# Kernel tuning notes

Hardware: AMD Instinct MI355X
Metric: run time of the kernel (lower is better)

The kernel has to match this reference:

```python
import jax, jax.numpy as jnp
import numpy as np

# Loihi neuron constants (from a typical slayerSNN network.yaml)
I_DECAY = 1024.0   # current decay (of 4096)
V_DECAY = 128.0    # voltage decay (of 4096)
THETA = 100.0      # firing threshold


def spike_loihi(x):
    """Loihi CUBA neuron dynamics over trailing time axis. x: [..., T] weighted input."""
    xT = jnp.moveaxis(x, -1, 0)  # [T, ...]
    a_i = (4096.0 - I_DECAY) / 4096.0
    a_v = (4096.0 - V_DECAY) / 4096.0

    def step(carry, xt):
        u, v = carry
        u = a_i * u + xt           # synaptic current
        v = a_v * v + u            # membrane voltage
        s = (v >= THETA).astype(x.dtype)
        v = v * (1.0 - s)          # reset on spike
        return (u, v), s

    z = jnp.zeros(xT.shape[1:], x.dtype)
    _, s = jax.lax.scan(step, (z, z), xT)
    return jnp.moveaxis(s, 0, -1)


def delay_shift(x):
    """Shift spikes by 1 timestep along last axis (slayer.delayShift(spike, 1))."""
    return jnp.concatenate([jnp.zeros_like(x[..., :1]), x[..., :-1]], axis=-1)


def conv_t(x, w):
    """Per-timestep 2D conv, padding 1. x: [N,C,H,W,T], w: [O,I,3,3]."""
    N, C, H, W, T = x.shape
    xt = jnp.transpose(x, (0, 4, 1, 2, 3)).reshape(N * T, C, H, W)
    y = jax.lax.conv_general_dilated(xt, w, (1, 1), [(1, 1), (1, 1)],
                                     dimension_numbers=('NCHW', 'OIHW', 'NCHW'))
    O = w.shape[0]
    return jnp.transpose(y.reshape(N, T, O, H, W), (0, 2, 3, 4, 1))


def sum_pool2(x, w):
    """slayer.pool(2): 2x2 sum-pool scaled by (loaded) scalar pool weight."""
    N, C, H, W, T = x.shape
    return x.reshape(N, C, H // 2, 2, W // 2, 2, T).sum(axis=(3, 5)) * w


def setup_inputs() -> dict:
    key = jax.random.key(0)
    ks = jax.random.split(key, 8)
    N, T = 16, 128
    spike = jax.random.bernoulli(ks[0], 0.1, (N, 2, 40, 40, T)).astype(jnp.float32)
    conv1_w = jax.random.normal(ks[1], (8, 2, 3, 3), jnp.float32) * 0.5
    conv2_w = jax.random.normal(ks[2], (16, 8, 3, 3), jnp.float32) * 0.05
    conv3_w = jax.random.normal(ks[3], (32, 16, 3, 3), jnp.float32) * 0.05
    fc1_w = jax.random.normal(ks[4], (512, 10 * 10 * 32), jnp.float32) * 0.02
    pool1_w = jnp.asarray(1.1, jnp.float32)
    pool2_w = jnp.asarray(1.1, jnp.float32)
    return {"spike": spike, "conv1_w": conv1_w, "conv2_w": conv2_w,
            "conv3_w": conv3_w, "pool1_w": pool1_w, "pool2_w": pool2_w,
            "fc1_w": fc1_w}


def reference(spike, conv1_w, conv2_w, conv3_w, pool1_w, pool2_w, fc1_w):
    x = spike_loihi(conv_t(spike, conv1_w * 20.0))    # weightScale=20
    x = delay_shift(x)
    x = spike_loihi(sum_pool2(x, pool1_w))
    x = delay_shift(x)
    x = spike_loihi(conv_t(x, conv2_w * 100.0))       # weightScale=100
    x = delay_shift(x)
    x = spike_loihi(sum_pool2(x, pool2_w))
    x = delay_shift(x)
    x = spike_loihi(conv_t(x, conv3_w * 100.0))       # weightScale=100
    N, T = x.shape[0], x.shape[-1]
    x = x.reshape(N, -1, 1, 1, T)                     # [N, 3200, 1, 1, T]
    x = delay_shift(x)
    x = spike_loihi(jnp.einsum('nchwt,oc->nohwt', x, fc1_w))
    x = delay_shift(x)
    return x
```

## Files before the change

kernel.cpp:

```cpp
#include <hip/hip_runtime.h>
#include <stdint.h>


#define T 128
#define AI 0.75f
#define AV 0.96875f
#define THETA 100.0f

typedef __attribute__((ext_vector_type(8))) short v8s;
typedef __attribute__((ext_vector_type(16))) float v16f;

__device__ __forceinline__ void neuron_step(float x, float& u, float& v, float& s) {
    u = AI * u + x;
    v = AV * v + u;
    s = (v >= THETA) ? 1.0f : 0.0f;
    v = v * (1.0f - s);
}

__global__ __launch_bounds__(256) void conv1_scan(
    const float* __restrict__ in, const float* __restrict__ cw,
    uint8_t* __restrict__ sout)
{
    __shared__ float ldsF[64 * 130];
    int bid0 = blockIdx.x;
    int bid = (bid0 & 7) * 400 + (bid0 >> 3);
    int wg = bid % 5;
    int hy = (bid / 5) % 40;
    int n  = bid / 200;
    int tid = threadIdx.x;
    int wxl = tid >> 5, tt = tid & 31, t0 = tt * 4;
    int wx = wg * 8 + wxl;

    float4 tap[18];
    #pragma unroll
    for (int c = 0; c < 2; c++)
      #pragma unroll
      for (int dh = 0; dh < 3; dh++)
        #pragma unroll
        for (int dw = 0; dw < 3; dw++) {
            int q = c * 9 + dh * 3 + dw;
            int hh = hy + dh - 1, ww = wx + dw - 1;
            bool ok = (hh >= 0) && (hh < 40) && (ww >= 0) && (ww < 40);
            tap[q] = ok ? *(const float4*)(in +
                (((size_t)(n * 2 + c) * 40 + hh) * 40 + ww) * T + t0)
                        : make_float4(0.f, 0.f, 0.f, 0.f);
        }

    #pragma unroll
    for (int o = 0; o < 8; o++) {
        const float* wp = cw + o * 18;
        float a0 = 0.f, a1 = 0.f, a2 = 0.f, a3 = 0.f;
        #pragma unroll
        for (int q = 0; q < 18; q++) {
            a0 += wp[q] * tap[q].x;  a1 += wp[q] * tap[q].y;
            a2 += wp[q] * tap[q].z;  a3 += wp[q] * tap[q].w;
        }
        float* xr = &ldsF[(o * 8 + wxl) * 130 + t0];
        xr[0] = a0 * 20.0f; xr[1] = a1 * 20.0f;
        xr[2] = a2 * 20.0f; xr[3] = a3 * 20.0f;
    }
    __syncthreads();
    if (tid < 64) {
        int o = tid >> 3, wxl2 = tid & 7;
        float u = 0.f, v = 0.f;
        uint32_t ob[32];
        const float* xr = &ldsF[tid * 130];
        #pragma unroll
        for (int tb = 0; tb < 32; tb++) {
            float s0, s1, s2, s3;
            neuron_step(xr[tb * 4 + 0], u, v, s0);
            neuron_step(xr[tb * 4 + 1], u, v, s1);
            neuron_step(xr[tb * 4 + 2], u, v, s2);
            neuron_step(xr[tb * 4 + 3], u, v, s3);
            ob[tb] = (uint32_t)s0 | ((uint32_t)s1 << 8) |
                     ((uint32_t)s2 << 16) | ((uint32_t)s3 << 24);
        }
        uint32_t* op = (uint32_t*)(sout +
            (((size_t)(n * 8 + o) * 40 + hy) * 40 + wg * 8 + wxl2) * T);
        #pragma unroll
        for (int k = 0; k < 8; k++)
            *(uint4*)&op[k * 4] =
                make_uint4(ob[k*4], ob[k*4+1], ob[k*4+2], ob[k*4+3]);
    }
}

template<int C, int HO, int WO>
__global__ __launch_bounds__(320) void pool_pad(
    const uint8_t* __restrict__ in, const float* __restrict__ pw_ptr,
    uint16_t* __restrict__ sP)
{
    constexpr int CB = 320 / C;
    constexpr int GP = (HO * WO) / CB;
    __shared__ uint8_t raw[320 * 132];
    uint32_t* ldsF = (uint32_t*)raw;
    uint8_t*  sbuf = raw;

    int bid = blockIdx.x;
    int grp = bid % GP, n = bid / GP;
    int tid = threadIdx.x;
    float pw = pw_ptr[0];

    float u = 0.f, v = 0.f;
    uint32_t ob[32];
    uint32_t carry = 0;

    #pragma unroll
    for (int tb = 0; tb < 2; tb++) {
        __syncthreads();
        #pragma unroll
        for (int k = 0; k < 4; k++) {
            int f = tid + k * 320;
            int row = f >> 2, q = f & 3;
            int c = row / CB, p = row % CB;
            int hw = grp * CB + p;
            int wx = hw % WO, hy = hw / WO;
            const uint8_t* p00 = in +
                (((size_t)(n * C + c) * (2 * HO) + 2 * hy) * (2 * WO) + 2 * wx) * T;
            int off = tb * 64 + q * 16;
            uint4 a = *(const uint4*)(p00 + off);
            uint4 b = *(const uint4*)(p00 + T + off);
            uint4 cc = *(const uint4*)(p00 + 2 * WO * T + off);
            uint4 d = *(const uint4*)(p00 + 2 * WO * T + T + off);
            *(uint4*)&ldsF[row * 20 + q * 4] =
                make_uint4(a.x + b.x + cc.x + d.x, a.y + b.y + cc.y + d.y,
                           a.z + b.z + cc.z + d.z, a.w + b.w + cc.w + d.w);
        }
        __syncthreads();
        #pragma unroll
        for (int q = 0; q < 4; q++) {
            uint4 w = *(const uint4*)&ldsF[tid * 20 + q * 4];
            uint32_t words[4] = {w.x, w.y, w.z, w.w};
            #pragma unroll
            for (int j = 0; j < 4; j++) {
                uint32_t cur = words[j];
                uint32_t del = (cur << 8) | carry;
                carry = cur >> 24;
                float s0, s1, s2, s3;
                neuron_step(pw * (float)(del & 0xffu),         u, v, s0);
                neuron_step(pw * (float)((del >> 8) & 0xffu),  u, v, s1);
                neuron_step(pw * (float)((del >> 16) & 0xffu), u, v, s2);
                neuron_step(pw * (float)((del >> 24) & 0xffu), u, v, s3);
                ob[tb * 16 + q * 4 + j] = (uint32_t)s0 | ((uint32_t)s1 << 8) |
                                          ((uint32_t)s2 << 16) | ((uint32_t)s3 << 24);
            }
        }
    }

    __syncthreads();
    #pragma unroll
    for (int j = 0; j < 32; j++)
        *(uint32_t*)&sbuf[tid * 132 + j * 4] = ob[j];
    __syncthreads();

    constexpr int CHK = CB * 128;
    #pragma unroll
    for (int k = 0; k < CHK / 320; k++) {
        int ci = k * 320 + tid;
        int p = ci >> 7, tau = ci & 127;
        int hw = grp * CB + p;
        int wx = hw % WO, hy = hw / WO;
        uint32_t wb[8];
        #pragma unroll
        for (int e = 0; e < 16; e += 2) {
            uint32_t lo = 0u, hi = 0u;
            if (tau >= 1) {
                if (e < C)     lo = sbuf[(e * CB + p) * 132 + tau - 1] ? 0x3F80u : 0u;
                if (e + 1 < C) hi = sbuf[((e + 1) * CB + p) * 132 + tau - 1] ? 0x3F80u : 0u;
            }
            wb[e >> 1] = lo | (hi << 16);
        }
        uint16_t* dst = sP + ((size_t)((n * (HO + 2) + hy + 1) * (WO + 2)
                                       + wx + 1)) * 2048 + tau * 16;
        *(uint4*)dst       = make_uint4(wb[0], wb[1], wb[2], wb[3]);
        *(uint4*)(dst + 8) = make_uint4(wb[4], wb[5], wb[6], wb[7]);
    }
}

template<int H, int W>
__global__ __launch_bounds__(256) void zero_halo(uint16_t* __restrict__ sP)
{
    constexpr int CELLS = (H + 2) * (W + 2);
    int bid = blockIdx.x;
    int cell = bid % CELLS;
    int hy = cell / (W + 2), wx = cell % (W + 2);
    if (hy >= 1 && hy <= H && wx >= 1 && wx <= W) return;
    *(uint4*)((uint8_t*)sP + (size_t)bid * 4096 + threadIdx.x * 16) =
        make_uint4(0u, 0u, 0u, 0u);
}

__global__ __launch_bounds__(64) void apack_w(
    const float* __restrict__ c2w, const float* __restrict__ c3w,
    uint16_t* __restrict__ apk)
{
    int bid = blockIdx.x;
    int conv = bid / 27;
    int plane = (bid % 27) / 9;
    int dlt = bid % 9;
    int lane = threadIdx.x;
    int o = lane & 31, chi = (lane >> 5) * 8;
    int CO = conv ? 32 : 16;
    int CI = conv ? 16 : 8;
    const float* Wp = conv ? c3w : c2w;
    uint32_t wb[4] = {0u, 0u, 0u, 0u};
    #pragma unroll
    for (int e = 0; e < 8; e++) {
        int c = chi + e;
        float w = (o < CO && c < CI) ? Wp[((size_t)o * CI + c) * 9 + dlt] : 0.f;
        uint32_t b0 = __float_as_uint(w);
        uint16_t hi = (uint16_t)(b0 >> 16);
        float r1 = w - __uint_as_float(b0 & 0xFFFF0000u);
        uint32_t b1 = __float_as_uint(r1);
        uint16_t md = (uint16_t)(b1 >> 16);
        float r2 = r1 - __uint_as_float(b1 & 0xFFFF0000u);
        uint16_t lo = (uint16_t)(__float_as_uint(r2) >> 16);
        uint32_t pv = (plane == 0) ? hi : ((plane == 1) ? md : lo);
        wb[e >> 1] |= pv << ((e & 1) * 16);
    }
    *(uint4*)(apk + ((size_t)conv * 27 + plane * 9 + dlt) * 512 + lane * 8) =
        make_uint4(wb[0], wb[1], wb[2], wb[3]);
}

template<int COUT, int PB, int H, int W>
__global__ __launch_bounds__(256, 2) void conv_scan_mfma(
    const uint16_t* __restrict__ sP, const uint16_t* __restrict__ apk,
    float scale, uint8_t* __restrict__ sout)
{
    __shared__ float ldsF[128 * 130];
    constexpr int HW = H * W;
    constexpr int GP = HW / PB;
    int per = (16 * GP) >> 3;
    int vbid = (blockIdx.x & 7) * per + (blockIdx.x >> 3);
    int n = vbid / GP, grp = vbid % GP;
    int tid = threadIdx.x;
    int wv = tid >> 6, lane = tid & 63;
    int l31 = lane & 31, lhi = lane >> 5;
    int t0 = wv * 32;

    const uint16_t* ap = apk + (size_t)lane * 8;
    v8s a0[9], a1[9], a2[9];
    #pragma unroll
    for (int d = 0; d < 9; d++) {
        a0[d] = *(const v8s*)(ap + d * 512);
        a1[d] = *(const v8s*)(ap + (9 + d) * 512);
        a2[d] = *(const v8s*)(ap + (18 + d) * 512);
    }

    #pragma unroll
    for (int p = 0; p < PB; p++) {
        int hw = grp * PB + p;
        int hy = hw / W, wx = hw % W;
        v8s bfr[9];
        #pragma unroll
        for (int d = 0; d < 9; d++) {
            int dh = d / 3, dw = d % 3;
            const uint16_t* src = sP
                + ((size_t)((n * (H + 2) + hy + dh) * (W + 2) + wx + dw)) * 2048
                + (t0 + l31) * 16 + lhi * 8;
            bfr[d] = *(const v8s*)src;
        }
        v16f ac0, ac1, ac2;
        #pragma unroll
        for (int e = 0; e < 16; e++) { ac0[e] = 0.f; ac1[e] = 0.f; ac2[e] = 0.f; }
        #pragma unroll
        for (int d = 0; d < 9; d++) {
            ac0 = __builtin_amdgcn_mfma_f32_32x32x16_bf16(a0[d], bfr[d], ac0, 0, 0, 0);
            ac1 = __builtin_amdgcn_mfma_f32_32x32x16_bf16(a1[d], bfr[d], ac1, 0, 0, 0);
            ac2 = __builtin_amdgcn_mfma_f32_32x32x16_bf16(a2[d], bfr[d], ac2, 0, 0, 0);
        }
        constexpr int NR = (COUT == 32) ? 16 : 8;
        #pragma unroll
        for (int r = 0; r < NR; r++) {
            int o = (r & 3) + 8 * (r >> 2) + 4 * lhi;
            ldsF[(o * PB + p) * 130 + t0 + l31] =
                (ac0[r] + ac1[r] + ac2[r]) * scale;
        }
    }
    __syncthreads();
    if (tid < 128) {
        int o = tid / PB, p = tid % PB;
        int hw = grp * PB + p;
        float u = 0.f, v = 0.f;
        uint32_t ob[32];
        const float* xr = &ldsF[tid * 130];
        #pragma unroll
        for (int tb = 0; tb < 32; tb++) {
            float2 xa = *(const float2*)(xr + tb * 4);
            float2 xb = *(const float2*)(xr + tb * 4 + 2);
            float s0, s1, s2, s3;
            neuron_step(xa.x, u, v, s0); neuron_step(xa.y, u, v, s1);
            neuron_step(xb.x, u, v, s2); neuron_step(xb.y, u, v, s3);
            ob[tb] = (uint32_t)s0 | ((uint32_t)s1 << 8) |
                     ((uint32_t)s2 << 16) | ((uint32_t)s3 << 24);
        }
        uint32_t* op = (uint32_t*)(sout + ((size_t)(n * COUT + o) * HW + hw) * 128);
        #pragma unroll
        for (int k = 0; k < 8; k++)
            *(uint4*)&op[k * 4] =
                make_uint4(ob[k*4], ob[k*4+1], ob[k*4+2], ob[k*4+3]);
    }
}

__global__ __launch_bounds__(256) void wsplit(
    const float* __restrict__ fw, uint16_t* __restrict__ bs)
{
    int i = blockIdx.x * 256 + threadIdx.x;
    float4 wv = *(const float4*)(fw + i * 4);
    float w4[4] = {wv.x, wv.y, wv.z, wv.w};
    uint16_t h[4], m[4], l[4];
    #pragma unroll
    for (int j = 0; j < 4; j++) {
        uint32_t b0 = __float_as_uint(w4[j]);
        h[j] = (uint16_t)(b0 >> 16);
        float r1 = w4[j] - __uint_as_float(b0 & 0xFFFF0000u);
        uint32_t b1 = __float_as_uint(r1);
        m[j] = (uint16_t)(b1 >> 16);
        float r2 = r1 - __uint_as_float(b1 & 0xFFFF0000u);
        l[j] = (uint16_t)(__float_as_uint(r2) >> 16);
    }
    *(ushort4*)(bs +       0 + i * 4) = make_ushort4(h[0], h[1], h[2], h[3]);
    *(ushort4*)(bs + 1638400 + i * 4) = make_ushort4(m[0], m[1], m[2], m[3]);
    *(ushort4*)(bs + 3276800 + i * 4) = make_ushort4(l[0], l[1], l[2], l[3]);
}

__global__ __launch_bounds__(256) void sT_bf16(
    const uint8_t* __restrict__ s5, uint16_t* __restrict__ At)
{
    __shared__ uint8_t tile[64 * 132];
    int bid = blockIdx.x;
    int n = bid / 50;
    int c0 = (bid % 50) * 64;
    int tid = threadIdx.x;
    {
        int row = tid >> 2, q = tid & 3;
        const uint8_t* src = s5 + ((size_t)(n * 3200 + c0 + row)) * T + q * 32;
        *(uint4*)&tile[row * 132 + q * 32]      = *(const uint4*)src;
        *(uint4*)&tile[row * 132 + q * 32 + 16] = *(const uint4*)(src + 16);
    }
    __syncthreads();
    int t = tid >> 1, half = tid & 1;
    uint32_t wb[16];
    if (t == 0) {
        #pragma unroll
        for (int j = 0; j < 16; j++) wb[j] = 0u;
    } else {
        #pragma unroll
        for (int j = 0; j < 16; j++) {
            uint32_t lo = tile[(half * 32 + 2 * j) * 132 + (t - 1)] ? 0x3F80u : 0u;
            uint32_t hi = tile[(half * 32 + 2 * j + 1) * 132 + (t - 1)] ? 0x3F80u : 0u;
            wb[j] = lo | (hi << 16);
        }
    }
    uint16_t* dst = At + ((size_t)(n * 128 + t)) * 3200 + c0 + half * 32;
    #pragma unroll
    for (int k = 0; k < 4; k++)
        *(uint4*)(dst + k * 8) = make_uint4(wb[k*4], wb[k*4+1], wb[k*4+2], wb[k*4+3]);
}

#define GLDS16(g, s) __builtin_amdgcn_global_load_lds( \
    (const __attribute__((address_space(1))) uint32_t*)(g), \
    (__attribute__((address_space(3))) uint32_t*)(s), 16, 0, 0)

__global__ __launch_bounds__(256, 2) void fc_gemm_mfma(
    const uint16_t* __restrict__ At,
    const uint16_t* __restrict__ Bs,
    float* __restrict__ ypart)
{
    __shared__ uint8_t lds[65536];
    int bid0 = blockIdx.x;
    int bid = (bid0 & 7) * 80 + (bid0 >> 3);
    int n  = bid & 15;
    int ob = (bid >> 4) & 3;
    int ks = bid >> 6;
    int o0 = ob * 128;
    int cbase = ks * 320;

    int tid = threadIdx.x;
    int w4 = tid >> 6;
    int wm = w4 >> 1;
    int wn = w4 & 1;
    int lane = tid & 63;
    int l31 = lane & 31;
    int lhi = lane >> 5;
    int rb = lane >> 3;
    int gsw = (lane & 7) ^ (rb & 7);

    v16f acc[2][2];
    #pragma unroll
    for (int mi = 0; mi < 2; mi++)
        #pragma unroll
        for (int ni = 0; ni < 2; ni++)
            #pragma unroll
            for (int e = 0; e < 16; e++) acc[mi][ni][e] = 0.0f;

    const uint16_t* Abase = At + (size_t)(n * 128) * 3200 + gsw * 8;

    for (int kc = 0; kc < 5; kc++) {
        int c0 = cbase + kc * 64;
        #pragma unroll
        for (int i = 0; i < 4; i++) {
            int cid = i * 4 + w4;
            const uint16_t* src = Abase + (size_t)(cid * 8 + rb) * 3200 + c0;
            GLDS16(src, lds + cid * 1024);
        }
        #pragma unroll
        for (int j = 0; j < 12; j++) {
            int cid = j * 4 + w4;
            int f0 = cid * 1024;
            int s = f0 >> 14;
            int r = ((f0 & 16383) >> 7) + rb;
            const uint16_t* src = Bs + (size_t)(s * 512 + o0 + r) * 3200
                                     + c0 + gsw * 8;
            GLDS16(src, lds + 16384 + f0);
        }
        __syncthreads();
        #pragma unroll
        for (int kf = 0; kf < 4; kf++) {
            int gc = kf * 2 + lhi;
            v8s av[2];
            #pragma unroll
            for (int mi = 0; mi < 2; mi++) {
                int t = wm * 64 + mi * 32 + l31;
                av[mi] = *(const v8s*)(lds + t * 128 + ((gc ^ (t & 7)) << 4));
            }
            #pragma unroll
            for (int s = 0; s < 3; s++) {
                #pragma unroll
                for (int ni = 0; ni < 2; ni++) {
                    int r = wn * 64 + ni * 32 + l31;
                    v8s bv = *(const v8s*)(lds + 16384 + s * 16384 + r * 128
                                           + ((gc ^ (r & 7)) << 4));
                    #pragma unroll
                    for (int mi = 0; mi < 2; mi++)
                        acc[mi][ni] = __builtin_amdgcn_mfma_f32_32x32x16_bf16(
                            av[mi], bv, acc[mi][ni], 0, 0, 0);
                }
            }
        }
        __syncthreads();
    }
    float* yp = ypart + (size_t)ks * 1048576 + (size_t)n * 65536;
    #pragma unroll
    for (int mi = 0; mi < 2; mi++)
        #pragma unroll
        for (int ni = 0; ni < 2; ni++) {
            int o = o0 + wn * 64 + ni * 32 + l31;
            #pragma unroll
            for (int r = 0; r < 16; r++) {
                int trow = wm * 64 + mi * 32 + (r & 3) + 8 * (r >> 2) + 4 * lhi;
                yp[trow * 512 + o] = acc[mi][ni][r];
            }
        }
}

__global__ __launch_bounds__(256) void fc_reduce(
    const float4* __restrict__ yp, float4* __restrict__ ys)
{
    int id = blockIdx.x * 256 + threadIdx.x;
    float4 x = yp[id];
    #pragma unroll
    for (int k = 1; k < 10; k++) {
        float4 y = yp[(size_t)k * 262144 + id];
        x.x += y.x; x.y += y.y; x.z += y.z; x.w += y.w;
    }
    ys[id] = x;
}

__global__ __launch_bounds__(64) void fc_scan(
    const float* __restrict__ ysum,
    float* __restrict__ out)
{
    int id = blockIdx.x * 64 + threadIdx.x;
    int o = id & 511;
    int n = id >> 9;
    float u = 0.f, v = 0.f;
    float prev = 0.f;
    for (int tb = 0; tb < T / 4; tb++) {
        float b0, b1, b2, b3;
        float x, s;
        x = ysum[(n * T + tb * 4 + 0) * 512 + o]; neuron_step(x, u, v, s); b0 = prev; prev = s;
        x = ysum[(n * T + tb * 4 + 1) * 512 + o]; neuron_step(x, u, v, s); b1 = prev; prev = s;
        x = ysum[(n * T + tb * 4 + 2) * 512 + o]; neuron_step(x, u, v, s); b2 = prev; prev = s;
        x = ysum[(n * T + tb * 4 + 3) * 512 + o]; neuron_step(x, u, v, s); b3 = prev; prev = s;
        *(float4*)&out[((size_t)(n * 512 + o)) * T + tb * 4] = make_float4(b0, b1, b2, b3);
    }
}

extern "C" void kernel_launch(void* const* d_in, const int* in_sizes, int n_in,
                              void* d_out, int out_size, void* d_ws, size_t ws_size,
                              hipStream_t stream) {
    const float* spike = (const float*)d_in[0];
    const float* c1w   = (const float*)d_in[1];
    const float* c2w   = (const float*)d_in[2];
    const float* c3w   = (const float*)d_in[3];
    const float* p1w   = (const float*)d_in[4];
    const float* p2w   = (const float*)d_in[5];
    const float* fcw   = (const float*)d_in[6];
    float* out = (float*)d_out;

    char* ws = (char*)d_ws;
    uint8_t*  s1    = (uint8_t*)(ws);
    uint16_t* Bs16  = (uint16_t*)(ws + 26214400);
    uint16_t* Apk   = (uint16_t*)(ws + 36044800);
    uint16_t* s2P   = (uint16_t*)(ws + 36100096);
    uint8_t*  s3    = (uint8_t*)(ws + 67819520);
    uint16_t* s4P   = (uint16_t*)(ws + 80926720);
    uint8_t*  s5    = (uint8_t*)(ws + 90363904);
    uint16_t* At16  = (uint16_t*)(ws + 96917504);
    float*    ypart = (float*)(ws + 110024704);
    float*    ysumb = (float*)(ws + 151967744);

    conv1_scan<<<3200, 256, 0, stream>>>(spike, c1w, s1);
    wsplit<<<1600, 256, 0, stream>>>(fcw, Bs16);
    apack_w<<<54, 64, 0, stream>>>(c2w, c3w, Apk);
    zero_halo<20, 20><<<16 * 484, 256, 0, stream>>>(s2P);
    zero_halo<10, 10><<<16 * 144, 256, 0, stream>>>(s4P);

    pool_pad<8, 20, 20><<<160, 320, 0, stream>>>(s1, p1w, s2P);
    conv_scan_mfma<16, 8, 20, 20><<<800, 256, 0, stream>>>(s2P, Apk, 100.0f, s3);

    pool_pad<16, 10, 10><<<80, 320, 0, stream>>>(s3, p2w, s4P);
    conv_scan_mfma<32, 4, 10, 10><<<400, 256, 0, stream>>>(s4P, Apk + 13824, 100.0f, s5);

    sT_bf16<<<800, 256, 0, stream>>>(s5, At16);
    fc_gemm_mfma<<<640, 256, 0, stream>>>(At16, Bs16, ypart);
    fc_reduce<<<1024, 256, 0, stream>>>((const float4*)ypart, (float4*)ysumb);
    fc_scan<<<128, 64, 0, stream>>>(ysumb, out);
}
```

Before: 259.0 us.

## Fuse prep kernels into one launch and widen FC GEMM to 8 waves

Merges the weight split, conv weight packing and halo zeroing into one prep kernel. Halo zeroing now launches blocks only for border cells instead of one block per cell with early exit. The FC GEMM moves from 256 to 512 threads per block, with each of the 8 waves computing a 64x32 tile instead of 64x64. This halves per-wave accumulators and spreads LDS staging across more waves. The aim is fewer launches, fewer idle blocks and more latency hiding in the GEMM, at the cost of more B-fragment LDS reads per MFMA.

```diff
diff --git a/kernel.cpp b/kernel.cpp
--- a/kernel.cpp
+++ b/kernel.cpp
@@ -176,48 +176,81 @@
     }
 }
 
-template<int H, int W>
-__global__ __launch_bounds__(256) void zero_halo(uint16_t* __restrict__ sP)
-{
-    constexpr int CELLS = (H + 2) * (W + 2);
+__global__ __launch_bounds__(256) void prep(
+    const float* __restrict__ fw, const float* __restrict__ c2w,
+    const float* __restrict__ c3w, uint16_t* __restrict__ bs,
+    uint16_t* __restrict__ apk, uint16_t* __restrict__ s2P,
+    uint16_t* __restrict__ s4P)
+{
     int bid = blockIdx.x;
-    int cell = bid % CELLS;
-    int hy = cell / (W + 2), wx = cell % (W + 2);
-    if (hy >= 1 && hy <= H && wx >= 1 && wx <= W) return;
-    *(uint4*)((uint8_t*)sP + (size_t)bid * 4096 + threadIdx.x * 16) =
-        make_uint4(0u, 0u, 0u, 0u);
-}
-
-__global__ __launch_bounds__(64) void apack_w(
-    const float* __restrict__ c2w, const float* __restrict__ c3w,
-    uint16_t* __restrict__ apk)
-{
-    int bid = blockIdx.x;
-    int conv = bid / 27;
-    int plane = (bid % 27) / 9;
-    int dlt = bid % 9;
-    int lane = threadIdx.x;
-    int o = lane & 31, chi = (lane >> 5) * 8;
-    int CO = conv ? 32 : 16;
-    int CI = conv ? 16 : 8;
-    const float* Wp = conv ? c3w : c2w;
-    uint32_t wb[4] = {0u, 0u, 0u, 0u};
-    #pragma unroll
-    for (int e = 0; e < 8; e++) {
-        int c = chi + e;
-        float w = (o < CO && c < CI) ? Wp[((size_t)o * CI + c) * 9 + dlt] : 0.f;
-        uint32_t b0 = __float_as_uint(w);
-        uint16_t hi = (uint16_t)(b0 >> 16);
-        float r1 = w - __uint_as_float(b0 & 0xFFFF0000u);
-        uint32_t b1 = __float_as_uint(r1);
-        uint16_t md = (uint16_t)(b1 >> 16);
-        float r2 = r1 - __uint_as_float(b1 & 0xFFFF0000u);
-        uint16_t lo = (uint16_t)(__float_as_uint(r2) >> 16);
-        uint32_t pv = (plane == 0) ? hi : ((plane == 1) ? md : lo);
-        wb[e >> 1] |= pv << ((e & 1) * 16);
-    }
-    *(uint4*)(apk + ((size_t)conv * 27 + plane * 9 + dlt) * 512 + lane * 8) =
-        make_uint4(wb[0], wb[1], wb[2], wb[3]);
+    int tid = threadIdx.x;
+    if (bid < 1600) {
+        int i = bid * 256 + tid;
+        float4 wv = *(const float4*)(fw + i * 4);
+        float w4[4] = {wv.x, wv.y, wv.z, wv.w};
+        uint16_t h[4], m[4], l[4];
+        #pragma unroll
+        for (int j = 0; j < 4; j++) {
+            uint32_t b0 = __float_as_uint(w4[j]);
+            h[j] = (uint16_t)(b0 >> 16);
+            float r1 = w4[j] - __uint_as_float(b0 & 0xFFFF0000u);
+            uint32_t b1 = __float_as_uint(r1);
+            m[j] = (uint16_t)(b1 >> 16);
+            float r2 = r1 - __uint_as_float(b1 & 0xFFFF0000u);
+            l[j] = (uint16_t)(__float_as_uint(r2) >> 16);
+        }
+        *(ushort4*)(bs +       0 + i * 4) = make_ushort4(h[0], h[1], h[2], h[3]);
+        *(ushort4*)(bs + 1638400 + i * 4) = make_ushort4(m[0], m[1], m[2], m[3]);
+        *(ushort4*)(bs + 3276800 + i * 4) = make_ushort4(l[0], l[1], l[2], l[3]);
+    } else if (bid < 1614) {
+        int unit = (bid - 1600) * 4 + (tid >> 6);
+        if (unit >= 54) return;
+        int conv = unit / 27;
+        int plane = (unit % 27) / 9;
+        int dlt = unit % 9;
+        int lane = tid & 63;
+        int o = lane & 31, chi = (lane >> 5) * 8;
+        int CO = conv ? 32 : 16;
+        int CI = conv ? 16 : 8;
+        const float* Wp = conv ? c3w : c2w;
+        uint32_t wb[4] = {0u, 0u, 0u, 0u};
+        #pragma unroll
+        for (int e = 0; e < 8; e++) {
+            int c = chi + e;
+            float w = (o < CO && c < CI) ? Wp[((size_t)o * CI + c) * 9 + dlt] : 0.f;
+            uint32_t b0 = __float_as_uint(w);
+            uint16_t hi = (uint16_t)(b0 >> 16);
+            float r1 = w - __uint_as_float(b0 & 0xFFFF0000u);
+            uint32_t b1 = __float_as_uint(r1);
+            uint16_t md = (uint16_t)(b1 >> 16);
+            float r2 = r1 - __uint_as_float(b1 & 0xFFFF0000u);
+            uint16_t lo = (uint16_t)(__float_as_uint(r2) >> 16);
+            uint32_t pv = (plane == 0) ? hi : ((plane == 1) ? md : lo);
+            wb[e >> 1] |= pv << ((e & 1) * 16);
+        }
+        *(uint4*)(apk + ((size_t)conv * 27 + plane * 9 + dlt) * 512 + lane * 8) =
+            make_uint4(wb[0], wb[1], wb[2], wb[3]);
+    } else {
+        int hid = bid - 1614;
+        uint8_t* dst;
+        if (hid < 1344) {
+            int n = hid / 84, r = hid % 84;
+            int hy, wx;
+            if (r < 22)      { hy = 0;  wx = r; }
+            else if (r < 44) { hy = 21; wx = r - 22; }
+            else { int r2 = r - 44; hy = 1 + (r2 >> 1); wx = (r2 & 1) ? 21 : 0; }
+            dst = (uint8_t*)s2P + ((size_t)(n * 484) + hy * 22 + wx) * 4096;
+        } else {
+            int h2 = hid - 1344;
+            int n = h2 / 44, r = h2 % 44;
+            int hy, wx;
+            if (r < 12)      { hy = 0;  wx = r; }
+            else if (r < 24) { hy = 11; wx = r - 12; }
+            else { int r2 = r - 24; hy = 1 + (r2 >> 1); wx = (r2 & 1) ? 11 : 0; }
+            dst = (uint8_t*)s4P + ((size_t)(n * 144) + hy * 12 + wx) * 4096;
+        }
+        *(uint4*)(dst + tid * 16) = make_uint4(0u, 0u, 0u, 0u);
+    }
 }
 
 template<int COUT, int PB, int H, int W>
@@ -300,28 +333,6 @@
     }
 }
 
-__global__ __launch_bounds__(256) void wsplit(
-    const float* __restrict__ fw, uint16_t* __restrict__ bs)
-{
-    int i = blockIdx.x * 256 + threadIdx.x;
-    float4 wv = *(const float4*)(fw + i * 4);
-    float w4[4] = {wv.x, wv.y, wv.z, wv.w};
-    uint16_t h[4], m[4], l[4];
-    #pragma unroll
-    for (int j = 0; j < 4; j++) {
-        uint32_t b0 = __float_as_uint(w4[j]);
-        h[j] = (uint16_t)(b0 >> 16);
-        float r1 = w4[j] - __uint_as_float(b0 & 0xFFFF0000u);
-        uint32_t b1 = __float_as_uint(r1);
-        m[j] = (uint16_t)(b1 >> 16);
-        float r2 = r1 - __uint_as_float(b1 & 0xFFFF0000u);
-        l[j] = (uint16_t)(__float_as_uint(r2) >> 16);
-    }
-    *(ushort4*)(bs +       0 + i * 4) = make_ushort4(h[0], h[1], h[2], h[3]);
-    *(ushort4*)(bs + 1638400 + i * 4) = make_ushort4(m[0], m[1], m[2], m[3]);
-    *(ushort4*)(bs + 3276800 + i * 4) = make_ushort4(l[0], l[1], l[2], l[3]);
-}
-
 __global__ __launch_bounds__(256) void sT_bf16(
     const uint8_t* __restrict__ s5, uint16_t* __restrict__ At)
 {
@@ -360,7 +371,7 @@
     (const __attribute__((address_space(1))) uint32_t*)(g), \
     (__attribute__((address_space(3))) uint32_t*)(s), 16, 0, 0)
 
-__global__ __launch_bounds__(256, 2) void fc_gemm_mfma(
+__global__ __launch_bounds__(512, 4) void fc_gemm_mfma(
     const uint16_t* __restrict__ At,
     const uint16_t* __restrict__ Bs,
     float* __restrict__ ypart)
@@ -375,36 +386,34 @@
     int cbase = ks * 320;
 
     int tid = threadIdx.x;
-    int w4 = tid >> 6;
-    int wm = w4 >> 1;
-    int wn = w4 & 1;
+    int w8 = tid >> 6;
+    int wm = w8 >> 2;
+    int wn = w8 & 3;
     int lane = tid & 63;
     int l31 = lane & 31;
     int lhi = lane >> 5;
     int rb = lane >> 3;
     int gsw = (lane & 7) ^ (rb & 7);
 
-    v16f acc[2][2];
+    v16f acc[2];
     #pragma unroll
     for (int mi = 0; mi < 2; mi++)
         #pragma unroll
-        for (int ni = 0; ni < 2; ni++)
-            #pragma unroll
-            for (int e = 0; e < 16; e++) acc[mi][ni][e] = 0.0f;
+        for (int e = 0; e < 16; e++) acc[mi][e] = 0.0f;
 
     const uint16_t* Abase = At + (size_t)(n * 128) * 3200 + gsw * 8;
 
     for (int kc = 0; kc < 5; kc++) {
         int c0 = cbase + kc * 64;
         #pragma unroll
-        for (int i = 0; i < 4; i++) {
-            int cid = i * 4 + w4;
+        for (int i = 0; i < 2; i++) {
+            int cid = i * 8 + w8;
             const uint16_t* src = Abase + (size_t)(cid * 8 + rb) * 3200 + c0;
             GLDS16(src, lds + cid * 1024);
         }
         #pragma unroll
-        for (int j = 0; j < 12; j++) {
-            int cid = j * 4 + w4;
+        for (int j = 0; j < 6; j++) {
+            int cid = j * 8 + w8;
             int f0 = cid * 1024;
             int s = f0 >> 14;
             int r = ((f0 & 16383) >> 7) + rb;
@@ -424,32 +433,27 @@
             }
             #pragma unroll
             for (int s = 0; s < 3; s++) {
+                int r = wn * 32 + l31;
+                v8s bv = *(const v8s*)(lds + 16384 + s * 16384 + r * 128
+                                       + ((gc ^ (r & 7)) << 4));
                 #pragma unroll
-                for (int ni = 0; ni < 2; ni++) {
-                    int r = wn * 64 + ni * 32 + l31;
-                    v8s bv = *(const v8s*)(lds + 16384 + s * 16384 + r * 128
-                                           + ((gc ^ (r & 7)) << 4));
-                    #pragma unroll
-                    for (int mi = 0; mi < 2; mi++)
-                        acc[mi][ni] = __builtin_amdgcn_mfma_f32_32x32x16_bf16(
-                            av[mi], bv, acc[mi][ni], 0, 0, 0);
-                }
+                for (int mi = 0; mi < 2; mi++)
+                    acc[mi] = __builtin_amdgcn_mfma_f32_32x32x16_bf16(
+                        av[mi], bv, acc[mi], 0, 0, 0);
             }
         }
         __syncthreads();
     }
     float* yp = ypart + (size_t)ks * 1048576 + (size_t)n * 65536;
-    #pragma unroll
-    for (int mi = 0; mi < 2; mi++)
-        #pragma unroll
-        for (int ni = 0; ni < 2; ni++) {
-            int o = o0 + wn * 64 + ni * 32 + l31;
-            #pragma unroll
-            for (int r = 0; r < 16; r++) {
-                int trow = wm * 64 + mi * 32 + (r & 3) + 8 * (r >> 2) + 4 * lhi;
-                yp[trow * 512 + o] = acc[mi][ni][r];
-            }
-        }
+    int o = o0 + wn * 32 + l31;
+    #pragma unroll
+    for (int mi = 0; mi < 2; mi++) {
+        #pragma unroll
+        for (int r = 0; r < 16; r++) {
+            int trow = wm * 64 + mi * 32 + (r & 3) + 8 * (r >> 2) + 4 * lhi;
+            yp[trow * 512 + o] = acc[mi][r];
+        }
+    }
 }
 
 __global__ __launch_bounds__(256) void fc_reduce(
@@ -509,11 +513,8 @@
     float*    ypart = (float*)(ws + 110024704);
     float*    ysumb = (float*)(ws + 151967744);
 
+    prep<<<3662, 256, 0, stream>>>(fcw, c2w, c3w, Bs16, Apk, s2P, s4P);
     conv1_scan<<<3200, 256, 0, stream>>>(spike, c1w, s1);
-    wsplit<<<1600, 256, 0, stream>>>(fcw, Bs16);
-    apack_w<<<54, 64, 0, stream>>>(c2w, c3w, Apk);
-    zero_halo<20, 20><<<16 * 484, 256, 0, stream>>>(s2P);
-    zero_halo<10, 10><<<16 * 144, 256, 0, stream>>>(s4P);
 
     pool_pad<8, 20, 20><<<160, 320, 0, stream>>>(s1, p1w, s2P);
     conv_scan_mfma<16, 8, 20, 20><<<800, 256, 0, stream>>>(s2P, Apk, 100.0f, s3);
@@ -522,7 +523,7 @@
     conv_scan_mfma<32, 4, 10, 10><<<400, 256, 0, stream>>>(s4P, Apk + 13824, 100.0f, s5);
 
     sT_bf16<<<800, 256, 0, stream>>>(s5, At16);
-    fc_gemm_mfma<<<640, 256, 0, stream>>>(At16, Bs16, ypart);
+    fc_gemm_mfma<<<640, 512, 0, stream>>>(At16, Bs16, ypart);
     fc_reduce<<<1024, 256, 0, stream>>>((const float4*)ypart, (float4*)ysumb);
     fc_scan<<<128, 64, 0, stream>>>(ysumb, out);
 }
```

New measurement: 316.2 us. 22.1% more time.
